# Optimization experiments

Hardware: AMD Instinct MI355X
Metric: run time of the kernel (lower is better)

The kernel has to match this reference:

```python
import jax, jax.numpy as jnp
import numpy as np

C_M, C_Z, NO_BINS = 256, 128, 15
MIN_BIN, MAX_BIN, INF = 3.25, 20.75, 1e8
LN_EPS = 1e-5


def _layer_norm(t, w, b):
    mu = jnp.mean(t, axis=-1, keepdims=True)
    var = jnp.var(t, axis=-1, keepdims=True)
    return (t - mu) * jax.lax.rsqrt(var + LN_EPS) * w + b


def setup_inputs() -> dict:
    key = jax.random.key(0)
    ks = jax.random.split(key, 8)
    B, N = 1, 768
    m = jax.random.normal(ks[0], (B, N, C_M), dtype=jnp.float32)
    z = jax.random.normal(ks[1], (B, N, N, C_Z), dtype=jnp.float32)
    # scale coords so pairwise distances span the 3.25-20.75 A bin range
    x = jax.random.normal(ks[2], (B, N, 3), dtype=jnp.float32) * 10.0
    seqs = jax.random.normal(ks[3], (B, N, 21), dtype=jnp.float32)
    lin_w = jax.random.normal(ks[4], (C_Z, NO_BINS), dtype=jnp.float32) * 0.1
    lin_b = jnp.zeros((C_Z,), dtype=jnp.float32)
    ln_m_w = jnp.ones((C_M,), dtype=jnp.float32)
    ln_m_b = jnp.zeros((C_M,), dtype=jnp.float32)
    ln_z_w = jnp.ones((C_Z,), dtype=jnp.float32)
    ln_z_b = jnp.zeros((C_Z,), dtype=jnp.float32)
    return {"m": m, "z": z, "x": x, "seqs": seqs,
            "lin_w": lin_w, "lin_b": lin_b,
            "ln_m_w": ln_m_w, "ln_m_b": ln_m_b,
            "ln_z_w": ln_z_w, "ln_z_b": ln_z_b}


def reference(m, z, x, seqs, lin_w, lin_b, ln_m_w, ln_m_b, ln_z_w, ln_z_b):
    # m update: LayerNorm only (track_seq_states=False, seqs unused)
    m_update = _layer_norm(m, ln_m_w, ln_m_b)

    bins = jnp.linspace(MIN_BIN, MAX_BIN, NO_BINS, dtype=x.dtype)
    sq_bins = bins ** 2
    upper = jnp.concatenate([sq_bins[1:], jnp.array([INF], dtype=x.dtype)])

    # pairwise squared distances [*, N, N, 1]
    diff = x[..., :, None, :] - x[..., None, :, :]
    d = jnp.sum(diff ** 2, axis=-1, keepdims=True)
    # one-hot distogram [*, N, N, no_bins] (strict inequalities, matching torch)
    oh = ((d > sq_bins) & (d < upper)).astype(x.dtype)
    # Linear(no_bins -> c_z)
    d_emb = jnp.einsum('...b,cb->...c', oh, lin_w) + lin_b

    z_update = d_emb + _layer_norm(z, ln_z_w, ln_z_b)
    return (m_update, z_update)
```

## Files before the change

kernel.cpp:

```cpp
#include <hip/hip_runtime.h>

#define LN_EPS 1e-5f
#define C_M 256
#define C_Z 128
#define NO_BINS 15

typedef float f4 __attribute__((ext_vector_type(4)));

__device__ __forceinline__ f4 f4zero() { f4 t = {0.f, 0.f, 0.f, 0.f}; return t; }

__global__ __launch_bounds__(256) void m_ln_kernel(
    const float* __restrict__ m, const float* __restrict__ w,
    const float* __restrict__ b, float* __restrict__ out, int nrows)
{
    const int wid  = threadIdx.x >> 6;
    const int lane = threadIdx.x & 63;
    const int row  = blockIdx.x * 4 + wid;
    if (row >= nrows) return;

    const f4 v = reinterpret_cast<const f4*>(m + (long long)row * C_M)[lane];
    float s  = v.x + v.y + v.z + v.w;
    float s2 = v.x * v.x + v.y * v.y + v.z * v.z + v.w * v.w;
#pragma unroll
    for (int msk = 1; msk < 64; msk <<= 1) {
        s  += __shfl_xor(s,  msk);
        s2 += __shfl_xor(s2, msk);
    }
    const float mu  = s * (1.0f / C_M);
    const float var = s2 * (1.0f / C_M) - mu * mu;
    const float inv = rsqrtf(var + LN_EPS);

    const f4 wv = reinterpret_cast<const f4*>(w)[lane];
    const f4 bv = reinterpret_cast<const f4*>(b)[lane];
    f4 o = (v - mu) * inv * wv + bv;
    reinterpret_cast<f4*>(out + (long long)row * C_M)[lane] = o;
}

__global__ __launch_bounds__(256) void bins_kernel(
    const float* __restrict__ x, signed char* __restrict__ bins, int N)
{
    __shared__ float sqb[16];
    if (threadIdx.x < 16) {
        const float bk = 3.25f + 1.25f * (float)threadIdx.x;
        sqb[threadIdx.x] = (threadIdx.x < NO_BINS) ? bk * bk : -1.0f;
    }
    __syncthreads();
    const int i = blockIdx.x;
    const int j = blockIdx.y * 256 + threadIdx.x;
    if (j >= N) return;

    const float dx = x[3 * i + 0] - x[3 * j + 0];
    const float dy = x[3 * i + 1] - x[3 * j + 1];
    const float dz = x[3 * i + 2] - x[3 * j + 2];
    const float d = __fadd_rn(__fadd_rn(__fmul_rn(dx, dx), __fmul_rn(dy, dy)),
                              __fmul_rn(dz, dz));
    int cnt = 0;
#pragma unroll
    for (int k = 0; k < NO_BINS; ++k) {
        const float bk = 3.25f + 1.25f * (float)k;
        cnt += (d > bk * bk) ? 1 : 0;
    }
    const bool valid = (cnt > 0) && (d < 1e8f) && (d != sqb[cnt]);
    bins[(long long)i * N + j] = valid ? (signed char)(cnt - 1) : (signed char)(-1);
}

__device__ __forceinline__ int inline_bin(const float* __restrict__ x,
                                          const float* sqb, long long r, int N)
{
    const int i = (int)(r / N);
    const int j = (int)(r - (long long)i * N);
    const float dx = x[3 * i + 0] - x[3 * j + 0];
    const float dy = x[3 * i + 1] - x[3 * j + 1];
    const float dz = x[3 * i + 2] - x[3 * j + 2];
    const float d = __fadd_rn(__fadd_rn(__fmul_rn(dx, dx), __fmul_rn(dy, dy)),
                              __fmul_rn(dz, dz));
    int cnt = 0;
#pragma unroll
    for (int k = 0; k < NO_BINS; ++k) {
        const float bk = 3.25f + 1.25f * (float)k;
        cnt += (d > bk * bk) ? 1 : 0;
    }
    const bool valid = (cnt > 0) && (d < 1e8f) && (d != sqb[cnt]);
    return valid ? cnt - 1 : -1;
}

template <bool PRECOMP>
__global__ __launch_bounds__(256) void z_fused(
    const float* __restrict__ z, const float* __restrict__ x,
    const float* __restrict__ lin_w, const float* __restrict__ lin_b,
    const float* __restrict__ w, const float* __restrict__ b,
    const signed char* __restrict__ bins, float* __restrict__ out, int N)
{
    __shared__ float lw[NO_BINS * C_Z];
    __shared__ float sqb[16];
    const int tid = threadIdx.x;
    for (int t = tid; t < NO_BINS * C_Z; t += 256) {
        const int c = t / NO_BINS;
        const int bin = t - c * NO_BINS;
        lw[bin * C_Z + c] = lin_w[t];
    }
    if (tid < 16) {
        const float bk = 3.25f + 1.25f * (float)tid;
        sqb[tid] = (tid < NO_BINS) ? bk * bk : -1.0f;
    }
    __syncthreads();

    const int half = tid >> 5;
    const int lane = tid & 31;

    const f4 wv = reinterpret_cast<const f4*>(w)[lane];
    f4 bv = reinterpret_cast<const f4*>(b)[lane];
    bv += reinterpret_cast<const f4*>(lin_b)[lane];

    const long long total  = (long long)N * N;
    const long long stride = (long long)gridDim.x * 8;

    for (long long r = (long long)blockIdx.x * 8 + half; r < total; r += 2 * stride) {
        const long long ra = r;
        const long long rb = r + stride;
        const bool hb = rb < total;

        const f4 va = reinterpret_cast<const f4*>(z + ra * C_Z)[lane];
        f4 vb = f4zero();
        if (hb) vb = reinterpret_cast<const f4*>(z + rb * C_Z)[lane];

        int bina, binb;
        if constexpr (PRECOMP) {
            bina = (int)bins[ra];
            binb = hb ? (int)bins[rb] : -1;
        } else {
            bina = inline_bin(x, sqb, ra, N);
            binb = hb ? inline_bin(x, sqb, rb, N) : -1;
        }

        f4 ea = f4zero(), eb = f4zero();
        if (bina >= 0) ea = reinterpret_cast<const f4*>(lw + bina * C_Z)[lane];
        if (binb >= 0) eb = reinterpret_cast<const f4*>(lw + binb * C_Z)[lane];

        float sa  = va.x + va.y + va.z + va.w;
        float s2a = va.x * va.x + va.y * va.y + va.z * va.z + va.w * va.w;
        float sb  = vb.x + vb.y + vb.z + vb.w;
        float s2b = vb.x * vb.x + vb.y * vb.y + vb.z * vb.z + vb.w * vb.w;
#pragma unroll
        for (int msk = 1; msk < 32; msk <<= 1) {
            sa  += __shfl_xor(sa,  msk);
            s2a += __shfl_xor(s2a, msk);
            sb  += __shfl_xor(sb,  msk);
            s2b += __shfl_xor(s2b, msk);
        }
        const float mua  = sa * (1.0f / C_Z);
        const float inva = rsqrtf(s2a * (1.0f / C_Z) - mua * mua + LN_EPS);
        const float mub  = sb * (1.0f / C_Z);
        const float invb = rsqrtf(s2b * (1.0f / C_Z) - mub * mub + LN_EPS);

        f4 oa = (va - mua) * inva * wv + bv + ea;
        __builtin_nontemporal_store(oa, reinterpret_cast<f4*>(out + ra * C_Z) + lane);
        if (hb) {
            f4 ob = (vb - mub) * invb * wv + bv + eb;
            __builtin_nontemporal_store(ob, reinterpret_cast<f4*>(out + rb * C_Z) + lane);
        }
    }
}

extern "C" void kernel_launch(void* const* d_in, const int* in_sizes, int n_in,
                              void* d_out, int out_size, void* d_ws, size_t ws_size,
                              hipStream_t stream) {
    const float* m      = (const float*)d_in[0];
    const float* z      = (const float*)d_in[1];
    const float* x      = (const float*)d_in[2];
    const float* lin_w  = (const float*)d_in[4];
    const float* lin_b  = (const float*)d_in[5];
    const float* ln_m_w = (const float*)d_in[6];
    const float* ln_m_b = (const float*)d_in[7];
    const float* ln_z_w = (const float*)d_in[8];
    const float* ln_z_b = (const float*)d_in[9];

    const int N = in_sizes[0] / C_M;
    float* out_m = (float*)d_out;
    float* out_z = out_m + (long long)N * C_M;

    m_ln_kernel<<<(N + 3) / 4, 256, 0, stream>>>(m, ln_m_w, ln_m_b, out_m, N);

    const long long rows = (long long)N * N;
    long long g = (rows + 15) / 16;
    if (g > 4608) g = 4608;
    const int z_blocks = (int)g;

    const bool pre = ws_size >= (size_t)rows;
    signed char* bins = (signed char*)d_ws;
    if (pre) {
        dim3 bg((unsigned)N, (unsigned)((N + 255) / 256));
        bins_kernel<<<bg, 256, 0, stream>>>(x, bins, N);
        z_fused<true><<<z_blocks, 256, 0, stream>>>(z, x, lin_w, lin_b,
                                                    ln_z_w, ln_z_b, bins, out_z, N);
    } else {
        z_fused<false><<<z_blocks, 256, 0, stream>>>(z, x, lin_w, lin_b,
                                                     ln_z_w, ln_z_b, nullptr, out_z, N);
    }
}
```

Measured before the change: 116.8 us.

## Fuse m LayerNorm, binning and z update into one kernel

```diff
diff --git a/kernel.cpp b/kernel.cpp
--- a/kernel.cpp
+++ b/kernel.cpp
@@ -9,46 +9,9 @@
 
 __device__ __forceinline__ f4 f4zero() { f4 t = {0.f, 0.f, 0.f, 0.f}; return t; }
 
-__global__ __launch_bounds__(256) void m_ln_kernel(
-    const float* __restrict__ m, const float* __restrict__ w,
-    const float* __restrict__ b, float* __restrict__ out, int nrows)
+__device__ __forceinline__ int bin_of(const float* __restrict__ x,
+                                      const float* sqb, int i, int j)
 {
-    const int wid  = threadIdx.x >> 6;
-    const int lane = threadIdx.x & 63;
-    const int row  = blockIdx.x * 4 + wid;
-    if (row >= nrows) return;
-
-    const f4 v = reinterpret_cast<const f4*>(m + (long long)row * C_M)[lane];
-    float s  = v.x + v.y + v.z + v.w;
-    float s2 = v.x * v.x + v.y * v.y + v.z * v.z + v.w * v.w;
-#pragma unroll
-    for (int msk = 1; msk < 64; msk <<= 1) {
-        s  += __shfl_xor(s,  msk);
-        s2 += __shfl_xor(s2, msk);
-    }
-    const float mu  = s * (1.0f / C_M);
-    const float var = s2 * (1.0f / C_M) - mu * mu;
-    const float inv = rsqrtf(var + LN_EPS);
-
-    const f4 wv = reinterpret_cast<const f4*>(w)[lane];
-    const f4 bv = reinterpret_cast<const f4*>(b)[lane];
-    f4 o = (v - mu) * inv * wv + bv;
-    reinterpret_cast<f4*>(out + (long long)row * C_M)[lane] = o;
-}
-
-__global__ __launch_bounds__(256) void bins_kernel(
-    const float* __restrict__ x, signed char* __restrict__ bins, int N)
-{
-    __shared__ float sqb[16];
-    if (threadIdx.x < 16) {
-        const float bk = 3.25f + 1.25f * (float)threadIdx.x;
-        sqb[threadIdx.x] = (threadIdx.x < NO_BINS) ? bk * bk : -1.0f;
-    }
-    __syncthreads();
-    const int i = blockIdx.x;
-    const int j = blockIdx.y * 256 + threadIdx.x;
-    if (j >= N) return;
-
     const float dx = x[3 * i + 0] - x[3 * j + 0];
     const float dy = x[3 * i + 1] - x[3 * j + 1];
     const float dz = x[3 * i + 2] - x[3 * j + 2];
@@ -60,36 +23,16 @@
         const float bk = 3.25f + 1.25f * (float)k;
         cnt += (d > bk * bk) ? 1 : 0;
     }
-    const bool valid = (cnt > 0) && (d < 1e8f) && (d != sqb[cnt]);
-    bins[(long long)i * N + j] = valid ? (signed char)(cnt - 1) : (signed char)(-1);
+    return ((cnt > 0) && (d < 1e8f) && (d != sqb[cnt])) ? cnt - 1 : -1;
 }
 
-__device__ __forceinline__ int inline_bin(const float* __restrict__ x,
-                                          const float* sqb, long long r, int N)
-{
-    const int i = (int)(r / N);
-    const int j = (int)(r - (long long)i * N);
-    const float dx = x[3 * i + 0] - x[3 * j + 0];
-    const float dy = x[3 * i + 1] - x[3 * j + 1];
-    const float dz = x[3 * i + 2] - x[3 * j + 2];
-    const float d = __fadd_rn(__fadd_rn(__fmul_rn(dx, dx), __fmul_rn(dy, dy)),
-                              __fmul_rn(dz, dz));
-    int cnt = 0;
-#pragma unroll
-    for (int k = 0; k < NO_BINS; ++k) {
-        const float bk = 3.25f + 1.25f * (float)k;
-        cnt += (d > bk * bk) ? 1 : 0;
-    }
-    const bool valid = (cnt > 0) && (d < 1e8f) && (d != sqb[cnt]);
-    return valid ? cnt - 1 : -1;
-}
-
-template <bool PRECOMP>
-__global__ __launch_bounds__(256) void z_fused(
+__global__ __launch_bounds__(256) void fused_kernel(
+    const float* __restrict__ m, const float* __restrict__ ln_m_w,
+    const float* __restrict__ ln_m_b, float* __restrict__ out_m, int m_rows,
     const float* __restrict__ z, const float* __restrict__ x,
     const float* __restrict__ lin_w, const float* __restrict__ lin_b,
-    const float* __restrict__ w, const float* __restrict__ b,
-    const signed char* __restrict__ bins, float* __restrict__ out, int N)
+    const float* __restrict__ ln_z_w, const float* __restrict__ ln_z_b,
+    float* __restrict__ out_z, int N, int di, int rem)
 {
     __shared__ float lw[NO_BINS * C_Z];
     __shared__ float sqb[16];
@@ -105,33 +48,59 @@
     }
     __syncthreads();
 
+    if ((int)blockIdx.x < ((m_rows + 3) >> 2)) {
+        const int wid    = tid >> 6;
+        const int lane64 = tid & 63;
+        const int row    = blockIdx.x * 4 + wid;
+        if (row < m_rows) {
+            const f4 v = reinterpret_cast<const f4*>(m + (long long)row * C_M)[lane64];
+            float s  = v.x + v.y + v.z + v.w;
+            float s2 = v.x * v.x + v.y * v.y + v.z * v.z + v.w * v.w;
+#pragma unroll
+            for (int msk = 1; msk < 64; msk <<= 1) {
+                s  += __shfl_xor(s,  msk);
+                s2 += __shfl_xor(s2, msk);
+            }
+            const float mu  = s * (1.0f / C_M);
+            const float inv = rsqrtf(s2 * (1.0f / C_M) - mu * mu + LN_EPS);
+            const f4 wv = reinterpret_cast<const f4*>(ln_m_w)[lane64];
+            const f4 bv = reinterpret_cast<const f4*>(ln_m_b)[lane64];
+            f4 o = (v - mu) * inv * wv + bv;
+            reinterpret_cast<f4*>(out_m + (long long)row * C_M)[lane64] = o;
+        }
+    }
+
     const int half = tid >> 5;
     const int lane = tid & 31;
 
-    const f4 wv = reinterpret_cast<const f4*>(w)[lane];
-    f4 bv = reinterpret_cast<const f4*>(b)[lane];
+    const f4 wv = reinterpret_cast<const f4*>(ln_z_w)[lane];
+    f4 bv = reinterpret_cast<const f4*>(ln_z_b)[lane];
     bv += reinterpret_cast<const f4*>(lin_b)[lane];
 
     const long long total  = (long long)N * N;
     const long long stride = (long long)gridDim.x * 8;
 
-    for (long long r = (long long)blockIdx.x * 8 + half; r < total; r += 2 * stride) {
+    long long r = (long long)blockIdx.x * 8 + half;
+    int i = (int)(r / N);
+    int j = (int)(r - (long long)i * N);
+
+    for (; r < total; r += 2 * stride) {
         const long long ra = r;
         const long long rb = r + stride;
         const bool hb = rb < total;
+
+        const int ia = i, ja = j;
+        int ib = i + di, jb = j + rem;
+        if (jb >= N) { jb -= N; ib += 1; }
+        i = ib + di; j = jb + rem;
+        if (j >= N) { j -= N; i += 1; }
 
         const f4 va = reinterpret_cast<const f4*>(z + ra * C_Z)[lane];
         f4 vb = f4zero();
         if (hb) vb = reinterpret_cast<const f4*>(z + rb * C_Z)[lane];
 
-        int bina, binb;
-        if constexpr (PRECOMP) {
-            bina = (int)bins[ra];
-            binb = hb ? (int)bins[rb] : -1;
-        } else {
-            bina = inline_bin(x, sqb, ra, N);
-            binb = hb ? inline_bin(x, sqb, rb, N) : -1;
-        }
+        const int bina = bin_of(x, sqb, ia, ja);
+        const int binb = hb ? bin_of(x, sqb, ib, jb) : -1;
 
         f4 ea = f4zero(), eb = f4zero();
         if (bina >= 0) ea = reinterpret_cast<const f4*>(lw + bina * C_Z)[lane];
@@ -154,10 +123,10 @@
         const float invb = rsqrtf(s2b * (1.0f / C_Z) - mub * mub + LN_EPS);
 
         f4 oa = (va - mua) * inva * wv + bv + ea;
-        __builtin_nontemporal_store(oa, reinterpret_cast<f4*>(out + ra * C_Z) + lane);
+        __builtin_nontemporal_store(oa, reinterpret_cast<f4*>(out_z + ra * C_Z) + lane);
         if (hb) {
             f4 ob = (vb - mub) * invb * wv + bv + eb;
-            __builtin_nontemporal_store(ob, reinterpret_cast<f4*>(out + rb * C_Z) + lane);
+            __builtin_nontemporal_store(ob, reinterpret_cast<f4*>(out_z + rb * C_Z) + lane);
         }
     }
 }
@@ -179,22 +148,18 @@
     float* out_m = (float*)d_out;
     float* out_z = out_m + (long long)N * C_M;
 
-    m_ln_kernel<<<(N + 3) / 4, 256, 0, stream>>>(m, ln_m_w, ln_m_b, out_m, N);
+    const int gcd8 = (N % 8 == 0) ? 8 : (N % 4 == 0) ? 4 : (N % 2 == 0) ? 2 : 1;
+    const int unit = N / gcd8;
+    int g = (4608 / unit) * unit;
+    if (g <= 0) g = unit;
+    const int mB = (N + 3) / 4;
+    if (g < mB) g = ((mB + unit - 1) / unit) * unit;
 
-    const long long rows = (long long)N * N;
-    long long g = (rows + 15) / 16;
-    if (g > 4608) g = 4608;
-    const int z_blocks = (int)g;
+    const long long stride = (long long)g * 8;
+    const int di  = (int)(stride / N);
+    const int rem = (int)(stride % N);
 
-    const bool pre = ws_size >= (size_t)rows;
-    signed char* bins = (signed char*)d_ws;
-    if (pre) {
-        dim3 bg((unsigned)N, (unsigned)((N + 255) / 256));
-        bins_kernel<<<bg, 256, 0, stream>>>(x, bins, N);
-        z_fused<true><<<z_blocks, 256, 0, stream>>>(z, x, lin_w, lin_b,
-                                                    ln_z_w, ln_z_b, bins, out_z, N);
-    } else {
-        z_fused<false><<<z_blocks, 256, 0, stream>>>(z, x, lin_w, lin_b,
-                                                     ln_z_w, ln_z_b, nullptr, out_z, N);
-    }
+    fused_kernel<<<g, 256, 0, stream>>>(m, ln_m_w, ln_m_b, out_m, N,
+                                        z, x, lin_w, lin_b, ln_z_w, ln_z_b,
+                                        out_z, N, di, rem);
 }
```

New measurement: 116.1 us. About the same (-0.6%).
